# Performance work log

Measured on AMD Instinct MI355X. Metric: run time of the kernel, lower is better.

Reference implementation:

```python
import jax, jax.numpy as jnp
import numpy as np

B, F, V = 64, 256, 128   # groups, frames/group, vecs/group (uniform ragged groups)
CF = 512                 # cross_feature


def setup_inputs() -> dict:
    key = jax.random.key(0)
    ks = jax.random.split(key, 18)
    p = lambda k, s: jax.random.normal(k, s, jnp.float32) * 0.02
    return {
        "metas": jax.random.uniform(ks[0], (B, 5), jnp.float32),
        "meta_indexs": jnp.arange(B),
        "frames": jax.random.normal(ks[1], (B * F, 600), jnp.float32),
        "frame_indexs": jnp.repeat(jnp.arange(B), F),
        "vecs": jax.random.normal(ks[2], (B * V, 768), jnp.float32),
        "vec_indexs": jnp.repeat(jnp.arange(B), V),
        "audios": jax.random.normal(ks[3], (B, 128), jnp.float32),
        "audio_indexs": jnp.arange(B),
        "Wfk": p(ks[4], (CF, 600)), "Wfv": p(ks[5], (CF, 600)),
        "Wvk": p(ks[6], (CF, 768)), "Wvv": p(ks[7], (CF, 768)),
        "Wav": p(ks[8], (CF, 128)),
        "Wff_f": p(ks[9], (2, CF, CF)),
        "Wff_v": p(ks[10], (2, CF, CF)),
        "Wff_a": p(ks[11], (2, CF, CF)),
        "Wout1": p(ks[12], (768, 3 * CF + 3)),
        "Wout2": p(ks[13], (512, 768)),
        "Wout3": p(ks[14], (64, 512)),
        "Wout4": p(ks[15], (1, 64)),
    }


def reference(metas, meta_indexs, frames, frame_indexs, vecs, vec_indexs,
              audios, audio_indexs, Wfk, Wfv, Wvk, Wvv, Wav,
              Wff_f, Wff_v, Wff_a, Wout1, Wout2, Wout3, Wout4):
    # groups are uniform: reshape ragged rows into [B, n, d] (indexes are
    # contiguous repeats per setup_inputs, so the mask-gathers become reshapes)
    b = audios.shape[0]
    fb = frames.reshape(b, -1, frames.shape[-1])   # [B,F,600]
    vb = vecs.reshape(b, -1, vecs.shape[-1])       # [B,V,768]
    relu = jax.nn.relu

    f_k = relu(jnp.einsum('bfd,cd->bfc', fb, Wfk))     # [B,F,CF]
    f_v = relu(jnp.einsum('bfd,cd->bfc', fb, Wfv))
    v_k = relu(jnp.einsum('bvd,cd->bvc', vb, Wvk))     # [B,V,CF]
    v_v = relu(jnp.einsum('bvd,cd->bvc', vb, Wvv))
    a_v = relu(audios @ Wav.T)                         # [B,CF]

    # torch: softmax(mm(k, q)) with no dim on an (N,1) tensor -> dim=1 -> ones,
    # so the initial "attended" queries are plain sums of the value projections.
    f_q_p = f_v.sum(axis=1)                            # [B,CF]
    v_q_p = v_v.sum(axis=1)
    a_q_p = a_v                                        # single audio row

    for i in range(2):
        attn_f = jax.nn.softmax(jnp.einsum('bfc,bc->bf', f_k, v_q_p) / CF, axis=1)
        f_c = jnp.einsum('bf,bfc->bc', attn_f, f_v)
        f_q_n = f_c @ Wff_f[i].T + f_q_p
        attn_v = jax.nn.softmax(jnp.einsum('bvc,bc->bv', v_k, v_q_p) / CF, axis=1)
        v_c = jnp.einsum('bv,bvc->bc', attn_v, v_v)
        v_q_n = v_c @ Wff_v[i].T + v_q_p
        # audio attention is softmax over a single element -> weight 1
        a_q_n = a_v @ Wff_a[i].T + a_q_p
        f_q_p, v_q_p, a_q_p = f_q_n, v_q_n, a_q_n      # dropout is dead code

    mean = a_q_p.mean(axis=1, keepdims=True)
    std = a_q_p.std(axis=1, keepdims=True, ddof=1)     # torch.std is unbiased
    na = (a_q_p - mean) / std

    goal = metas[:, 1:2] / 1500.0
    dura = metas[:, 3:4] - metas[:, 2:3]
    dura = jnp.where(dura > 8000.0, 100.0, dura) / 100.0
    create = metas[:, 4:5] / 5.0

    feats = jnp.concatenate([f_q_p, v_q_p, na, goal, create, dura], axis=1)  # [B,1539]
    h = relu(feats @ Wout1.T)
    h = relu(h @ Wout2.T)
    h = relu(h @ Wout3.T)
    out = jax.nn.sigmoid(h @ Wout4.T)                  # [B,1]
    return out[:, 0]
```

## Files before the change

kernel.cpp:

```cpp
#include <hip/hip_runtime.h>
#include <hip/hip_bf16.h>

typedef __attribute__((ext_vector_type(4))) float f32x4;
typedef __attribute__((ext_vector_type(8))) __bf16 bf16x8;
typedef __attribute__((ext_vector_type(8))) unsigned short us8;
typedef __attribute__((ext_vector_type(4))) unsigned int u32x4;

#define LDS_AS __attribute__((address_space(3)))
#define GLB_AS __attribute__((address_space(1)))

__device__ __forceinline__ unsigned short f2bf(float f) {
    unsigned u = __builtin_bit_cast(unsigned, f);
    return (unsigned short)((u + 0x7FFFu + ((u >> 16) & 1u)) >> 16);
}
__device__ __forceinline__ float bf2f(unsigned short h) {
    return __builtin_bit_cast(float, (unsigned)h << 16);
}
__device__ __forceinline__ void cp16(const void* g, void* l) {
    __builtin_amdgcn_global_load_lds((const GLB_AS unsigned int*)g,
                                     (LDS_AS unsigned int*)l, 16, 0, 0);
}

#define NPREPB 544
#define NTOT 557056
__global__ __launch_bounds__(256) void prep_kernel(
    const float* __restrict__ Wfk, const float* __restrict__ Wfv,
    const float* __restrict__ Wvk, const float* __restrict__ Wvv,
    const float* __restrict__ Wout1, const float* __restrict__ audios, const float* __restrict__ Wav,
    unsigned short* __restrict__ wf, unsigned short* __restrict__ wv,
    float* __restrict__ W1p, float* __restrict__ hacc, float* __restrict__ qz,
    float* __restrict__ a_v, float* __restrict__ a_q_p)
{
    __shared__ float aud[128];
    const int t = threadIdx.x;
    if (blockIdx.x >= NPREPB) {
        const int b = blockIdx.x - NPREPB;
        if (t < 128) aud[t] = audios[b * 128 + t];
        __syncthreads();
        #pragma unroll
        for (int cc = 0; cc < 2; ++cc) {
            int c = 2 * t + cc;
            const float* wr = Wav + (size_t)c * 128;
            float s = 0.f;
            #pragma unroll
            for (int k4 = 0; k4 < 32; ++k4) {
                f32x4 wvv = *(const f32x4*)(wr + k4 * 4);
                s += wvv[0] * aud[k4 * 4] + wvv[1] * aud[k4 * 4 + 1]
                   + wvv[2] * aud[k4 * 4 + 2] + wvv[3] * aud[k4 * 4 + 3];
            }
            s = s > 0.f ? s : 0.f;
            a_v[b * 512 + c] = s;
            a_q_p[b * 512 + c] = s;
        }
        return;
    }
    for (int i = blockIdx.x * 256 + t; i < NTOT; i += NPREPB * 256) {
        int idx = i;
        if (idx < 77824) {
            int row = idx / 76, k = (idx - row * 76) * 8;
            const float* src = row < 512 ? Wfk + (size_t)row * 600 : Wfv + (size_t)(row - 512) * 600;
            us8 o = {0, 0, 0, 0, 0, 0, 0, 0};
            if (k < 600) {
                f32x4 v0 = *(const f32x4*)(src + k);
                f32x4 v1 = *(const f32x4*)(src + k + 4);
                o[0] = f2bf(v0[0]); o[1] = f2bf(v0[1]); o[2] = f2bf(v0[2]); o[3] = f2bf(v0[3]);
                o[4] = f2bf(v1[0]); o[5] = f2bf(v1[1]); o[6] = f2bf(v1[2]); o[7] = f2bf(v1[3]);
            }
            *(us8*)(wf + (size_t)row * 608 + k) = o;
            continue;
        }
        idx -= 77824;
        if (idx < 98304) {
            int row = idx / 96, k = (idx - row * 96) * 8;
            const float* src = (row < 512 ? Wvk + (size_t)row * 768
                                          : Wvv + (size_t)(row - 512) * 768) + k;
            f32x4 v0 = *(const f32x4*)src;
            f32x4 v1 = *(const f32x4*)(src + 4);
            us8 o = {f2bf(v0[0]), f2bf(v0[1]), f2bf(v0[2]), f2bf(v0[3]),
                     f2bf(v1[0]), f2bf(v1[1]), f2bf(v1[2]), f2bf(v1[3])};
            *(us8*)(wv + (size_t)row * 768 + k) = o;
            continue;
        }
        idx -= 98304;
        if (idx < 344064) {
            int r = idx / 448, k = (idx - r * 448) * 4;
            f32x4 o;
            #pragma unroll
            for (int j = 0; j < 4; ++j) {
                int kk = k + j;
                o[j] = kk < 1539 ? Wout1[(size_t)r * 1539 + kk] : 0.f;
            }
            *(f32x4*)(W1p + (size_t)r * 1792 + k) = o;
            continue;
        }
        idx -= 344064;
        if (idx < 20480) {
            f32x4 z = {0, 0, 0, 0};
            *(f32x4*)(hacc + (size_t)idx * 4) = z;
            continue;
        }
        idx -= 20480;
        {
            f32x4 z = {0, 0, 0, 0};
            *(f32x4*)(qz + (size_t)idx * 4) = z;
        }
    }
}

__global__ __launch_bounds__(256) void gemm_fused(
    const float* __restrict__ Afp, int Kreal,
    const unsigned short* __restrict__ B,
    unsigned short* __restrict__ C, int Kp, float* __restrict__ qout, int gshift)
{
    __shared__ alignas(16) unsigned short sA[2 * 4096];
    __shared__ alignas(16) unsigned short sB[2 * 4096];
    const int t = threadIdx.x;
    const int w = t >> 6, l = t & 63;
    const int nwg = gridDim.x;
    const int swz = (blockIdx.x & 7) * (nwg >> 3) + (blockIdx.x >> 3);
    const int bm = swz >> 3, bn = swz & 7;
    const int m0 = bm << 7, n0 = bn << 7;

    const int srow = t >> 2, sk0 = (t & 3) << 3;
    const unsigned short* gB = B + (size_t)(n0 + srow) * Kp + sk0;
    const int arow = t >> 1, ac0 = (t & 1) << 4;
    const float* gA = Afp + (size_t)(m0 + arow) * Kreal + ac0;

    const int wr = w >> 1, wc = w & 1;
    const int ksteps = Kp >> 5;

    f32x4 av[4];
    {
        char* lB = (char*)sB + w * 1024;
        cp16(gB, lB);
        cp16(gB + (size_t)64 * Kp, lB + 4096);
        #pragma unroll
        for (int j = 0; j < 4; ++j) {
            int c = ac0 + j * 4;
            av[j] = (c < Kreal) ? *(const f32x4*)(gA + j * 4) : f32x4{0.f, 0.f, 0.f, 0.f};
        }
        unsigned short* dA = sA + arow * 32 + ac0;
        #pragma unroll
        for (int h = 0; h < 2; ++h) {
            us8 o;
            #pragma unroll
            for (int e = 0; e < 8; ++e) {
                float f = av[h * 2 + (e >> 2)][e & 3];
                o[e] = __builtin_bit_cast(unsigned short, __float2bfloat16(f));
            }
            *(us8*)(dA + h * 8) = o;
        }
    }
    __syncthreads();

    f32x4 acc[4][4] = {};
    int cur = 0;
    for (int kt = 0; kt < ksteps; ++kt) {
        const bool more = (kt + 1 < ksteps);
        if (more) {
            const unsigned short* gb = gB + (kt + 1) * 32;
            char* lB = (char*)sB + (cur ^ 1) * 8192 + w * 1024;
            cp16(gb, lB);
            cp16(gb + (size_t)64 * Kp, lB + 4096);
            #pragma unroll
            for (int j = 0; j < 4; ++j) {
                int c = (kt + 1) * 32 + ac0 + j * 4;
                av[j] = (c < Kreal) ? *(const f32x4*)(gA + (kt + 1) * 32 + j * 4)
                                    : f32x4{0.f, 0.f, 0.f, 0.f};
            }
        }
        const unsigned short* pA = sA + cur * 4096 + (wr * 64 + (l & 15)) * 32 + ((l >> 4) << 3);
        const unsigned short* pB = sB + cur * 4096 + (wc * 64 + (l & 15)) * 32 + ((l >> 4) << 3);
        bf16x8 af[4], bfr[4];
        #pragma unroll
        for (int i = 0; i < 4; ++i) {
            af[i]  = *(const bf16x8*)(pA + i * 512);
            bfr[i] = *(const bf16x8*)(pB + i * 512);
        }
        #pragma unroll
        for (int mi = 0; mi < 4; ++mi)
            #pragma unroll
            for (int ni = 0; ni < 4; ++ni)
                acc[mi][ni] = __builtin_amdgcn_mfma_f32_16x16x32_bf16(af[mi], bfr[ni], acc[mi][ni], 0, 0, 0);
        if (more) {
            unsigned short* dA = sA + (cur ^ 1) * 4096 + arow * 32 + ac0;
            #pragma unroll
            for (int h = 0; h < 2; ++h) {
                us8 o;
                #pragma unroll
                for (int e = 0; e < 8; ++e) {
                    float f = av[h * 2 + (e >> 2)][e & 3];
                    o[e] = __builtin_bit_cast(unsigned short, __float2bfloat16(f));
                }
                *(us8*)(dA + h * 8) = o;
            }
        }
        __syncthreads();
        cur ^= 1;
    }

    const int crow0 = m0 + wr * 64 + ((l >> 4) << 2);
    const int ccol0 = n0 + wc * 64 + (l & 15);
    #pragma unroll
    for (int mi = 0; mi < 4; ++mi)
        #pragma unroll
        for (int ni = 0; ni < 4; ++ni)
            #pragma unroll
            for (int j = 0; j < 4; ++j) {
                float v = acc[mi][ni][j];
                v = v > 0.f ? v : 0.f;
                C[(size_t)(crow0 + mi * 16 + j) * 1024 + (ccol0 + ni * 16)] = f2bf(v);
            }
    if (n0 >= 512) {
        const int g = m0 >> gshift;
        float csum[4];
        #pragma unroll
        for (int ni = 0; ni < 4; ++ni) {
            float s = 0.f;
            #pragma unroll
            for (int mi = 0; mi < 4; ++mi)
                #pragma unroll
                for (int j = 0; j < 4; ++j)
                    s += fmaxf(acc[mi][ni][j], 0.f);
            s += __shfl_xor(s, 16, 64);
            s += __shfl_xor(s, 32, 64);
            csum[ni] = s;
        }
        if (l < 16) {
            #pragma unroll
            for (int ni = 0; ni < 4; ++ni)
                atomicAdd(&qout[g * 512 + (ccol0 - 512) + ni * 16], csum[ni]);
        }
    }
}

__global__ __launch_bounds__(256) void scores_kernel(
    const unsigned short* __restrict__ Cf, const unsigned short* __restrict__ Cv,
    const float* __restrict__ v_q_p, float* __restrict__ sbuf, float* __restrict__ fvz)
{
    const int t = threadIdx.x, bid = blockIdx.x;
    if (bid < 64) {
        f32x4 z = {0, 0, 0, 0};
        ((f32x4*)fvz)[bid * 256 + t] = z;
    }
    const int w = t >> 6, l = t & 63;
    int frame, g, soff;
    const unsigned short* X;
    if (bid < 4096) { frame = bid * 4 + w; g = frame >> 8; X = Cf; soff = 0; }
    else            { frame = (bid - 4096) * 4 + w; g = frame >> 7; X = Cv; soff = 16384; }
    const float* vq = v_q_p + g * 512 + l * 8;
    f32x4 q0 = *(const f32x4*)vq;
    f32x4 q1 = *(const f32x4*)(vq + 4);
    u32x4 u = *(const u32x4*)(X + (size_t)frame * 1024 + l * 8);
    float acc = q0[0] * bf2f((unsigned short)(u[0] & 0xffff)) + q0[1] * bf2f((unsigned short)(u[0] >> 16))
              + q0[2] * bf2f((unsigned short)(u[1] & 0xffff)) + q0[3] * bf2f((unsigned short)(u[1] >> 16))
              + q1[0] * bf2f((unsigned short)(u[2] & 0xffff)) + q1[1] * bf2f((unsigned short)(u[2] >> 16))
              + q1[2] * bf2f((unsigned short)(u[3] & 0xffff)) + q1[3] * bf2f((unsigned short)(u[3] >> 16));
    #pragma unroll
    for (int m = 1; m < 64; m <<= 1) acc += __shfl_xor(acc, m, 64);
    if (l == 0) sbuf[soff + frame] = acc * (1.f / 512.f);
}

__global__ __launch_bounds__(256) void pv_kernel(
    const unsigned short* __restrict__ Cf, const unsigned short* __restrict__ Cv,
    const float* __restrict__ sbuf, float* __restrict__ fc, float* __restrict__ vc)
{
    __shared__ float ws[256];
    __shared__ float red[256];
    const int t = threadIdx.x, bid = blockIdx.x;
    int g, chunk, NF, soff;
    const unsigned short* X;
    float* outp;
    if (bid < 512) { g = bid >> 3; chunk = bid & 7; NF = 256; X = Cf; soff = g * 256; outp = fc; }
    else { int b2 = bid - 512; g = b2 >> 2; chunk = b2 & 3; NF = 128; X = Cv; soff = 16384 + g * 128; outp = vc; }
    float s = (t < NF) ? sbuf[soff + t] : -1e30f;
    red[t] = s;
    __syncthreads();
    for (int st = 128; st > 0; st >>= 1) { if (t < st) red[t] = fmaxf(red[t], red[t + st]); __syncthreads(); }
    float m = red[0];
    __syncthreads();
    float e = (t < NF) ? __expf(s - m) : 0.f;
    ws[t] = e;
    red[t] = e;
    __syncthreads();
    for (int st = 128; st > 0; st >>= 1) { if (t < st) red[t] += red[t + st]; __syncthreads(); }
    float inv = 1.f / red[0];
    const int f0 = g * NF + chunk * 32;
    const unsigned int* q = (const unsigned int*)X + (size_t)f0 * 512 + 256 + t;
    float s0 = 0.f, s1 = 0.f;
    #pragma unroll 4
    for (int f = 0; f < 32; ++f) {
        float a = ws[chunk * 32 + f];
        unsigned u = q[(size_t)f * 512];
        s0 += a * bf2f((unsigned short)(u & 0xffff));
        s1 += a * bf2f((unsigned short)(u >> 16));
    }
    atomicAdd(&outp[g * 512 + 2 * t],     s0 * inv);
    atomicAdd(&outp[g * 512 + 2 * t + 1], s1 * inv);
}

__device__ __forceinline__ void gemv_body(
    const float* __restrict__ X, int ldx, int dorelu,
    const float* __restrict__ W, int ldw, float* __restrict__ Y, int ldy,
    int nc, int kc, int bc)
{
    __shared__ float xs[4096];
    const int t = threadIdx.x;
    #pragma unroll
    for (int j = 0; j < 16; ++j) {
        int idx = t + j * 256;
        float v = X[(size_t)(bc * 32 + (idx >> 7)) * ldx + kc * 128 + (idx & 127)];
        xs[idx] = dorelu ? (v > 0.f ? v : 0.f) : v;
    }
    __syncthreads();
    const int r = t & 63, bg = t >> 6;
    const int row = nc * 64 + r;
    const float* wrow = W + (size_t)row * ldw + kc * 128;
    float acc[8] = {};
    #pragma unroll 8
    for (int k4 = 0; k4 < 32; ++k4) {
        f32x4 wvv = *(const f32x4*)(wrow + k4 * 4);
        #pragma unroll
        for (int bb = 0; bb < 8; ++bb) {
            f32x4 xv = *(const f32x4*)(xs + (bg * 8 + bb) * 128 + k4 * 4);
            acc[bb] += wvv[0] * xv[0] + wvv[1] * xv[1] + wvv[2] * xv[2] + wvv[3] * xv[3];
        }
    }
    #pragma unroll
    for (int bb = 0; bb < 8; ++bb)
        atomicAdd(&Y[(size_t)(bc * 32 + bg * 8 + bb) * ldy + row], acc[bb]);
}

__global__ __launch_bounds__(256) void update_kernel(
    const float* __restrict__ Wff_f, const float* __restrict__ Wff_v, const float* __restrict__ Wff_a,
    int iter, const float* __restrict__ fc, const float* __restrict__ vc, const float* __restrict__ a_v,
    float* __restrict__ f_q_p, float* __restrict__ v_q_p, float* __restrict__ a_q_p)
{
    int id = blockIdx.x;
    const int op = id >> 6; id &= 63;
    const int nc = id & 7, kc = (id >> 3) & 3, bc = id >> 5;
    const float* W = (op == 0 ? Wff_f : op == 1 ? Wff_v : Wff_a) + (size_t)iter * 262144;
    const float* X = op == 0 ? fc : op == 1 ? vc : a_v;
    float* Y = op == 0 ? f_q_p : op == 1 ? v_q_p : a_q_p;
    gemv_body(X, 512, 0, W, 512, Y, 512, nc, kc, bc);
}

__global__ __launch_bounds__(256) void gemvb_kernel(
    const float* __restrict__ X, int ldx, int dorelu,
    const float* __restrict__ W, int ldw, float* __restrict__ Y, int ldy,
    int NC, int KC)
{
    int bid = blockIdx.x;
    const int nc = bid % NC; bid /= NC;
    const int kc = bid % KC;
    const int bc = bid / KC;
    gemv_body(X, ldx, dorelu, W, ldw, Y, ldy, nc, kc, bc);
}

__global__ __launch_bounds__(512) void normfeats_kernel(
    const float* __restrict__ a_q_p, const float* __restrict__ f_q_p, const float* __restrict__ v_q_p,
    const float* __restrict__ metas, float* __restrict__ feats)
{
    __shared__ float red[512];
    const int t = threadIdx.x, b = blockIdx.x;
    float a = a_q_p[b * 512 + t];
    red[t] = a;
    __syncthreads();
    for (int s = 256; s > 0; s >>= 1) { if (t < s) red[t] += red[t + s]; __syncthreads(); }
    float mean = red[0] * (1.f / 512.f);
    __syncthreads();
    float d = a - mean;
    red[t] = d * d;
    __syncthreads();
    for (int s = 256; s > 0; s >>= 1) { if (t < s) red[t] += red[t + s]; __syncthreads(); }
    float sd = sqrtf(red[0] * (1.f / 511.f));
    float* fr = feats + (size_t)b * 1792;
    fr[t]        = f_q_p[b * 512 + t];
    fr[512 + t]  = v_q_p[b * 512 + t];
    fr[1024 + t] = d / sd;
    if (t < 256) {
        float v = 0.f;
        if (t == 0) v = metas[b * 5 + 1] * (1.f / 1500.f);
        else if (t == 1) v = metas[b * 5 + 4] * 0.2f;
        else if (t == 2) {
            float du = metas[b * 5 + 3] - metas[b * 5 + 2];
            v = (du > 8000.f ? 100.f : du) * 0.01f;
        }
        fr[1536 + t] = v;
    }
}

__global__ __launch_bounds__(256) void mlp34_kernel(
    const float* __restrict__ h2acc, const float* __restrict__ W3, const float* __restrict__ W4,
    float* __restrict__ out)
{
    __shared__ float xs[512];
    __shared__ float part[256];
    __shared__ float h3[64];
    const int t = threadIdx.x, b = blockIdx.x;
    {
        float v0 = h2acc[(size_t)b * 512 + t];
        float v1 = h2acc[(size_t)b * 512 + 256 + t];
        xs[t] = v0 > 0.f ? v0 : 0.f;
        xs[256 + t] = v1 > 0.f ? v1 : 0.f;
    }
    __syncthreads();
    const int r = t & 63, q = t >> 6;
    const float* wrow = W3 + (size_t)r * 512 + q * 128;
    float acc = 0.f;
    #pragma unroll 8
    for (int k4 = 0; k4 < 32; ++k4) {
        f32x4 wvv = *(const f32x4*)(wrow + k4 * 4);
        f32x4 xv  = *(const f32x4*)(xs + q * 128 + k4 * 4);
        acc += wvv[0] * xv[0] + wvv[1] * xv[1] + wvv[2] * xv[2] + wvv[3] * xv[3];
    }
    part[t] = acc;
    __syncthreads();
    if (t < 64) {
        float h = part[t] + part[t + 64] + part[t + 128] + part[t + 192];
        h3[t] = h > 0.f ? h : 0.f;
    }
    __syncthreads();
    if (t < 64) {
        float v = h3[t] * W4[t];
        #pragma unroll
        for (int m = 1; m < 64; m <<= 1) v += __shfl_xor(v, m, 64);
        if (t == 0) out[b] = 1.f / (1.f + __expf(-v));
    }
}

extern "C" void kernel_launch(void* const* d_in, const int* in_sizes, int n_in,
                              void* d_out, int out_size, void* d_ws, size_t ws_size,
                              hipStream_t stream)
{
    const float* metas  = (const float*)d_in[0];
    const float* frames = (const float*)d_in[2];
    const float* vecs   = (const float*)d_in[4];
    const float* audios = (const float*)d_in[6];
    const float* Wfk   = (const float*)d_in[8];
    const float* Wfv   = (const float*)d_in[9];
    const float* Wvk   = (const float*)d_in[10];
    const float* Wvv   = (const float*)d_in[11];
    const float* Wav   = (const float*)d_in[12];
    const float* Wff_f = (const float*)d_in[13];
    const float* Wff_v = (const float*)d_in[14];
    const float* Wff_a = (const float*)d_in[15];
    const float* Wout1 = (const float*)d_in[16];
    const float* Wout2 = (const float*)d_in[17];
    const float* Wout3 = (const float*)d_in[18];
    const float* Wout4 = (const float*)d_in[19];
    float* out = (float*)d_out;

    char* p = (char*)d_ws;
    auto alloc = [&](size_t n) { char* r = p; p += (n + 255) & ~(size_t)255; return r; };
    unsigned short* wf  = (unsigned short*)alloc(1024ull * 608 * 2);
    unsigned short* wv  = (unsigned short*)alloc(1024ull * 768 * 2);
    unsigned short* Cf  = (unsigned short*)alloc(16384ull * 1024 * 2);
    unsigned short* Cv  = (unsigned short*)alloc(8192ull * 1024 * 2);
    float* W1p   = (float*)alloc(768ull * 1792 * 4);
    float* feats = (float*)alloc(64ull * 1792 * 4);
    float* qbuf  = (float*)alloc(2ull * 64 * 512 * 4);
    float* f_q_p = qbuf;
    float* v_q_p = qbuf + 64 * 512;
    float* a_q_p = (float*)alloc(64ull * 512 * 4);
    float* a_v   = (float*)alloc(64ull * 512 * 4);
    float* fvc   = (float*)alloc(2ull * 64 * 512 * 4);
    float* fcb   = fvc;
    float* vcb   = fvc + 64 * 512;
    float* hacc  = (float*)alloc(81920ull * 4);
    float* h1acc = hacc;
    float* h2acc = hacc + 64 * 768;
    float* sbuf  = (float*)alloc(24576ull * 4);

    prep_kernel<<<NPREPB + 64, 256, 0, stream>>>(Wfk, Wfv, Wvk, Wvv, Wout1, audios, Wav,
                                                 wf, wv, W1p, hacc, qbuf, a_v, a_q_p);
    gemm_fused<<<1024, 256, 0, stream>>>(frames, 600, wf, Cf, 608, f_q_p, 8);
    gemm_fused<<<512, 256, 0, stream>>>(vecs, 768, wv, Cv, 768, v_q_p, 7);
    for (int i = 0; i < 2; ++i) {
        scores_kernel<<<6144, 256, 0, stream>>>(Cf, Cv, v_q_p, sbuf, fvc);
        pv_kernel<<<768, 256, 0, stream>>>(Cf, Cv, sbuf, fcb, vcb);
        update_kernel<<<192, 256, 0, stream>>>(Wff_f, Wff_v, Wff_a, i, fcb, vcb, a_v,
                                               f_q_p, v_q_p, a_q_p);
    }
    normfeats_kernel<<<64, 512, 0, stream>>>(a_q_p, f_q_p, v_q_p, metas, feats);
    gemvb_kernel<<<336, 256, 0, stream>>>(feats, 1792, 0, W1p, 1792, h1acc, 768, 12, 14);
    gemvb_kernel<<<96, 256, 0, stream>>>(h1acc, 768, 1, Wout2, 768, h2acc, 512, 8, 6);
    mlp34_kernel<<<64, 256, 0, stream>>>(h2acc, Wout3, Wout4, out);
}
```

Baseline: 191.7 us.

## Stage fp32 A tiles directly to LDS via async copies, convert to bf16 on read

```diff
diff --git a/kernel.cpp b/kernel.cpp
--- a/kernel.cpp
+++ b/kernel.cpp
@@ -22,14 +22,14 @@
 }
 
 #define NPREPB 544
-#define NTOT 557056
+#define NTOT 557072
 __global__ __launch_bounds__(256) void prep_kernel(
     const float* __restrict__ Wfk, const float* __restrict__ Wfv,
     const float* __restrict__ Wvk, const float* __restrict__ Wvv,
     const float* __restrict__ Wout1, const float* __restrict__ audios, const float* __restrict__ Wav,
     unsigned short* __restrict__ wf, unsigned short* __restrict__ wv,
     float* __restrict__ W1p, float* __restrict__ hacc, float* __restrict__ qz,
-    float* __restrict__ a_v, float* __restrict__ a_q_p)
+    float* __restrict__ a_v, float* __restrict__ a_q_p, float* __restrict__ zbuf)
 {
     __shared__ float aud[128];
     const int t = threadIdx.x;
@@ -100,20 +100,26 @@
             continue;
         }
         idx -= 20480;
+        if (idx < 16384) {
+            f32x4 z = {0, 0, 0, 0};
+            *(f32x4*)(qz + (size_t)idx * 4) = z;
+            continue;
+        }
+        idx -= 16384;
         {
             f32x4 z = {0, 0, 0, 0};
-            *(f32x4*)(qz + (size_t)idx * 4) = z;
+            *(f32x4*)(zbuf + (size_t)idx * 4) = z;
         }
     }
 }
 
 __global__ __launch_bounds__(256) void gemm_fused(
-    const float* __restrict__ Afp, int Kreal,
-    const unsigned short* __restrict__ B,
-    unsigned short* __restrict__ C, int Kp, float* __restrict__ qout, int gshift)
-{
-    __shared__ alignas(16) unsigned short sA[2 * 4096];
-    __shared__ alignas(16) unsigned short sB[2 * 4096];
+    const float* __restrict__ Afp, int Kreal, int ktiles,
+    const unsigned short* __restrict__ B, int Kp,
+    unsigned short* __restrict__ C, float* __restrict__ qout, int gshift,
+    const float* __restrict__ zbuf)
+{
+    __shared__ alignas(16) char lds[2][24576];
     const int t = threadIdx.x;
     const int w = t >> 6, l = t & 63;
     const int nwg = gridDim.x;
@@ -121,80 +127,60 @@
     const int bm = swz >> 3, bn = swz & 7;
     const int m0 = bm << 7, n0 = bn << 7;
 
-    const int srow = t >> 2, sk0 = (t & 3) << 3;
-    const unsigned short* gB = B + (size_t)(n0 + srow) * Kp + sk0;
-    const int arow = t >> 1, ac0 = (t & 1) << 4;
-    const float* gA = Afp + (size_t)(m0 + arow) * Kreal + ac0;
+    const int arow = t >> 3;
+    const int acd = t & 7;
+    const int brow = t >> 2, bc0 = (t & 3) << 3;
 
     const int wr = w >> 1, wc = w & 1;
-    const int ksteps = Kp >> 5;
-
-    f32x4 av[4];
-    {
-        char* lB = (char*)sB + w * 1024;
-        cp16(gB, lB);
-        cp16(gB + (size_t)64 * Kp, lB + 4096);
-        #pragma unroll
-        for (int j = 0; j < 4; ++j) {
-            int c = ac0 + j * 4;
-            av[j] = (c < Kreal) ? *(const f32x4*)(gA + j * 4) : f32x4{0.f, 0.f, 0.f, 0.f};
-        }
-        unsigned short* dA = sA + arow * 32 + ac0;
-        #pragma unroll
-        for (int h = 0; h < 2; ++h) {
-            us8 o;
-            #pragma unroll
-            for (int e = 0; e < 8; ++e) {
-                float f = av[h * 2 + (e >> 2)][e & 3];
-                o[e] = __builtin_bit_cast(unsigned short, __float2bfloat16(f));
-            }
-            *(us8*)(dA + h * 8) = o;
-        }
-    }
+
+    const int rA = wr * 64 + (l & 15);
+    const int keyA = l & 7;
+    const int c2 = (l >> 4) << 1;
+    const int pa0 = (c2 ^ keyA) << 2;
+    const int pa1 = ((c2 + 1) ^ keyA) << 2;
+    const int pBoff = ((wc * 64 + (l & 15)) << 5) + ((l >> 4) << 3);
+
+    auto stage = [&](int buf, int kt) {
+        char* base = lds[buf];
+        #pragma unroll
+        for (int q = 0; q < 4; ++q) {
+            int row = q * 32 + arow;
+            int sc = acd ^ (row & 7);
+            int colf = kt * 32 + sc * 4;
+            const float* src = (colf < Kreal)
+                ? (Afp + (size_t)(m0 + row) * Kreal + colf) : zbuf;
+            cp16(src, base + q * 4096 + w * 1024);
+        }
+        const unsigned short* gb = B + (size_t)(n0 + brow) * Kp + bc0 + kt * 32;
+        cp16(gb, base + 16384 + w * 1024);
+        cp16(gb + (size_t)64 * Kp, base + 16384 + 4096 + w * 1024);
+    };
+
+    stage(0, 0);
     __syncthreads();
 
     f32x4 acc[4][4] = {};
     int cur = 0;
-    for (int kt = 0; kt < ksteps; ++kt) {
-        const bool more = (kt + 1 < ksteps);
-        if (more) {
-            const unsigned short* gb = gB + (kt + 1) * 32;
-            char* lB = (char*)sB + (cur ^ 1) * 8192 + w * 1024;
-            cp16(gb, lB);
-            cp16(gb + (size_t)64 * Kp, lB + 4096);
-            #pragma unroll
-            for (int j = 0; j < 4; ++j) {
-                int c = (kt + 1) * 32 + ac0 + j * 4;
-                av[j] = (c < Kreal) ? *(const f32x4*)(gA + (kt + 1) * 32 + j * 4)
-                                    : f32x4{0.f, 0.f, 0.f, 0.f};
-            }
-        }
-        const unsigned short* pA = sA + cur * 4096 + (wr * 64 + (l & 15)) * 32 + ((l >> 4) << 3);
-        const unsigned short* pB = sB + cur * 4096 + (wc * 64 + (l & 15)) * 32 + ((l >> 4) << 3);
+    for (int kt = 0; kt < ktiles; ++kt) {
+        if (kt + 1 < ktiles) stage(cur ^ 1, kt + 1);
+        const float* fA = (const float*)(lds[cur]);
+        const unsigned short* sB = (const unsigned short*)(lds[cur] + 16384);
         bf16x8 af[4], bfr[4];
         #pragma unroll
         for (int i = 0; i < 4; ++i) {
-            af[i]  = *(const bf16x8*)(pA + i * 512);
-            bfr[i] = *(const bf16x8*)(pB + i * 512);
+            const float* rp = fA + (size_t)(rA + i * 16) * 32;
+            f32x4 lo = *(const f32x4*)(rp + pa0);
+            f32x4 hi = *(const f32x4*)(rp + pa1);
+            us8 o = {f2bf(lo[0]), f2bf(lo[1]), f2bf(lo[2]), f2bf(lo[3]),
+                     f2bf(hi[0]), f2bf(hi[1]), f2bf(hi[2]), f2bf(hi[3])};
+            af[i] = __builtin_bit_cast(bf16x8, o);
+            bfr[i] = *(const bf16x8*)(sB + pBoff + i * 512);
         }
         #pragma unroll
         for (int mi = 0; mi < 4; ++mi)
             #pragma unroll
             for (int ni = 0; ni < 4; ++ni)
                 acc[mi][ni] = __builtin_amdgcn_mfma_f32_16x16x32_bf16(af[mi], bfr[ni], acc[mi][ni], 0, 0, 0);
-        if (more) {
-            unsigned short* dA = sA + (cur ^ 1) * 4096 + arow * 32 + ac0;
-            #pragma unroll
-            for (int h = 0; h < 2; ++h) {
-                us8 o;
-                #pragma unroll
-                for (int e = 0; e < 8; ++e) {
-                    float f = av[h * 2 + (e >> 2)][e & 3];
-                    o[e] = __builtin_bit_cast(unsigned short, __float2bfloat16(f));
-                }
-                *(us8*)(dA + h * 8) = o;
-            }
-        }
         __syncthreads();
         cur ^= 1;
     }
@@ -471,11 +457,12 @@
     float* h1acc = hacc;
     float* h2acc = hacc + 64 * 768;
     float* sbuf  = (float*)alloc(24576ull * 4);
+    float* zbuf  = (float*)alloc(64ull * 4);
 
     prep_kernel<<<NPREPB + 64, 256, 0, stream>>>(Wfk, Wfv, Wvk, Wvv, Wout1, audios, Wav,
-                                                 wf, wv, W1p, hacc, qbuf, a_v, a_q_p);
-    gemm_fused<<<1024, 256, 0, stream>>>(frames, 600, wf, Cf, 608, f_q_p, 8);
-    gemm_fused<<<512, 256, 0, stream>>>(vecs, 768, wv, Cv, 768, v_q_p, 7);
+                                                 wf, wv, W1p, hacc, qbuf, a_v, a_q_p, zbuf);
+    gemm_fused<<<1024, 256, 0, stream>>>(frames, 600, 19, wf, 608, Cf, f_q_p, 8, zbuf);
+    gemm_fused<<<512, 256, 0, stream>>>(vecs, 768, 24, wv, 768, Cv, v_q_p, 7, zbuf);
     for (int i = 0; i < 2; ++i) {
         scores_kernel<<<6144, 256, 0, stream>>>(Cf, Cv, v_q_p, sbuf, fvc);
         pv_kernel<<<768, 256, 0, stream>>>(Cf, Cv, sbuf, fcb, vcb);
```

Result: faster. 178.1 us (-7.1%).
